# Kernel optimization log

Hardware: AMD Instinct MI355X
Metric: run time of the kernel (lower is better)

## Reference

```python
import jax, jax.numpy as jnp
import numpy as np

N_NODES = 100000
N_EDGES = 1600000
IN_CH = 128
OUT_CH = 32
HEADS = 2
NEG_SLOPE = 0.2  # GATv2Conv default negative_slope


def setup_inputs() -> dict:
    key = jax.random.key(0)
    ks = jax.random.split(key, 6)
    x = jax.random.normal(ks[0], (N_NODES, IN_CH), dtype=jnp.float32)
    edge_index = jax.random.randint(ks[1], (2, N_EDGES), 0, N_NODES, dtype=jnp.int64)
    s_in = 1.0 / np.sqrt(IN_CH)
    Wl = jax.random.normal(ks[2], (IN_CH, HEADS * OUT_CH), dtype=jnp.float32) * s_in  # lin_l weight
    Wr = jax.random.normal(ks[3], (IN_CH, HEADS * OUT_CH), dtype=jnp.float32) * s_in  # lin_r weight
    bl = jnp.zeros((HEADS * OUT_CH,), dtype=jnp.float32)
    br = jnp.zeros((HEADS * OUT_CH,), dtype=jnp.float32)
    att = jax.random.normal(ks[4], (HEADS, OUT_CH), dtype=jnp.float32) * (1.0 / np.sqrt(OUT_CH))
    bias = jnp.zeros((OUT_CH,), dtype=jnp.float32)  # output bias (concat=False -> size out_channels)
    return {"x": x, "Wl": Wl, "bl": bl, "Wr": Wr, "br": br, "att": att, "bias": bias,
            "edge_index": edge_index}


def _gatv2_layer(x, Wl, bl, Wr, br, att, bias, edge_index):
    N = x.shape[0]
    H, C = att.shape
    # add self loops (GATv2Conv default add_self_loops=True)
    loops = jnp.arange(N, dtype=edge_index.dtype)
    src = jnp.concatenate([edge_index[0], loops])  # [E+N] message sources j
    dst = jnp.concatenate([edge_index[1], loops])  # [E+N] message targets i
    # per-node linear transforms (share_weights=False)
    xl = (x @ Wl + bl).reshape(N, H, C)
    xr = (x @ Wr + br).reshape(N, H, C)
    # GATv2 dynamic attention: a^T LeakyReLU(xl[j] + xr[i])
    h = xl[src] + xr[dst]                                   # [E, H, C]
    e = jnp.einsum('ehc,hc->eh', jax.nn.leaky_relu(h, NEG_SLOPE), att)  # [E, H]
    # segment softmax over incoming edges of each target node
    m = jax.ops.segment_max(e, dst, num_segments=N)         # [N, H]
    a = jnp.exp(e - m[dst])
    denom = jax.ops.segment_sum(a, dst, num_segments=N)     # [N, H]
    alpha = a / (denom[dst] + 1e-16)                        # [E, H]
    # weighted scatter-add of source messages
    out = jax.ops.segment_sum(alpha[:, :, None] * xl[src], dst, num_segments=N)  # [N, H, C]
    out = out.mean(axis=1) + bias                           # concat=False -> head mean
    return jax.nn.silu(out)                                 # activation='silu'


def reference(x, Wl, bl, Wr, br, att, bias, edge_index):
    return _gatv2_layer(x, Wl, bl, Wr, br, att, bias, edge_index)
```

## Files before the change

### kernel.cpp

```cpp
#include <hip/hip_runtime.h>
#include <math.h>

#define BSH 9
#define BMASK ((1 << BSH) - 1)
#define CAP 12288
#define ACH 2048

typedef unsigned int uint;
typedef __attribute__((ext_vector_type(8))) short bf16x8;
typedef __attribute__((ext_vector_type(4))) float f32x4;
typedef __attribute__((ext_vector_type(2))) float f32x2;

static __device__ __forceinline__ unsigned short f2bf(float f) {
    uint u = __float_as_uint(f);
    return (unsigned short)((u + 0x7fffu + ((u >> 16) & 1u)) >> 16);
}

static __device__ __forceinline__ bf16x8 pack8(float4 a, float4 b) {
    uint p0, p1, p2, p3;
    asm("v_cvt_pk_bf16_f32 %0, %1, %2" : "=v"(p0) : "v"(a.x), "v"(a.y));
    asm("v_cvt_pk_bf16_f32 %0, %1, %2" : "=v"(p1) : "v"(a.z), "v"(a.w));
    asm("v_cvt_pk_bf16_f32 %0, %1, %2" : "=v"(p2) : "v"(b.x), "v"(b.y));
    asm("v_cvt_pk_bf16_f32 %0, %1, %2" : "=v"(p3) : "v"(b.z), "v"(b.w));
    uint4 u = make_uint4(p0, p1, p2, p3);
    return *(bf16x8*)&u;
}

static __device__ __forceinline__ f32x2 dec2(uint u) {
    f32x2 r;
    r.x = __uint_as_float(u << 16);
    r.y = __uint_as_float(u & 0xffff0000u);
    return r;
}

static __device__ __forceinline__ f32x2 abs2(f32x2 h) {
    f32x2 r;
    r.x = __uint_as_float(__float_as_uint(h.x) & 0x7fffffffu);
    r.y = __uint_as_float(__float_as_uint(h.y) & 0x7fffffffu);
    return r;
}

static __device__ __forceinline__ float qsum(float p) {
    p += __uint_as_float(__builtin_amdgcn_mov_dpp(__float_as_uint(p), 0xB1, 0xF, 0xF, true));
    p += __uint_as_float(__builtin_amdgcn_mov_dpp(__float_as_uint(p), 0x4E, 0xF, 0xF, true));
    return p;
}

__global__ __launch_bounds__(256) void k_prep(const float* __restrict__ Wl,
                                              const float* __restrict__ Wr,
                                              unsigned short* __restrict__ Wt) {
    __shared__ unsigned short s[16][130];
    int b = blockIdx.x;
    int t = threadIdx.x;
#pragma unroll
    for (int i = 0; i < 8; ++i) {
        int idx = i * 256 + t;
        int kl = idx >> 7;
        int n  = idx & 127;
        int k  = b * 16 + kl;
        float v = (n < 64) ? Wl[k * 64 + n] : Wr[k * 64 + (n - 64)];
        s[kl][n] = f2bf(v);
    }
    __syncthreads();
#pragma unroll
    for (int i = 0; i < 2; ++i) {
        int idx = i * 256 + t;
        int n  = idx >> 2;
        int kg = idx & 3;
        ushort4 v;
        v.x = s[kg * 4 + 0][n]; v.y = s[kg * 4 + 1][n];
        v.z = s[kg * 4 + 2][n]; v.w = s[kg * 4 + 3][n];
        *(ushort4*)(Wt + n * 128 + b * 16 + kg * 4) = v;
    }
}

static __device__ __forceinline__ void gemm_body(
        const float* __restrict__ x, const unsigned short* __restrict__ Wt,
        const float* __restrict__ bl, const float* __restrict__ br,
        unsigned short* __restrict__ xlh, float* __restrict__ xr, int N, int bid)
{
    const int t = threadIdx.x;
    const int base = bid * 128;
    const int w = t >> 6;
    const int lo = t & 15;
    const int hi = (t & 63) >> 4;
    int row0 = base + w * 32 + lo;
    int row1 = row0 + 16;
    const float4* x40 = (const float4*)x + (size_t)(row0 < N ? row0 : N - 1) * 32;
    const float4* x41 = (const float4*)x + (size_t)(row1 < N ? row1 : N - 1) * 32;

    f32x4 acc[2][8];
#pragma unroll
    for (int f = 0; f < 2; ++f)
#pragma unroll
        for (int j = 0; j < 8; ++j)
            acc[f][j] = (f32x4){0.f, 0.f, 0.f, 0.f};

#pragma unroll
    for (int ks = 0; ks < 4; ++ks) {
        int f4 = ks * 8 + hi * 2;
        int kofs = ks * 32 + hi * 8;
        bf16x8 av[2], bv[8];
        av[0] = pack8(x40[f4], x40[f4 + 1]);
        av[1] = pack8(x41[f4], x41[f4 + 1]);
#pragma unroll
        for (int j = 0; j < 8; ++j) {
            int nn = j * 16 + lo;
            bv[j] = *(const bf16x8*)(Wt + nn * 128 + kofs);
        }
#pragma unroll
        for (int f = 0; f < 2; ++f)
#pragma unroll
            for (int j = 0; j < 8; ++j)
                acc[f][j] = __builtin_amdgcn_mfma_f32_16x16x32_bf16(av[f], bv[j], acc[f][j], 0, 0, 0);
    }

#pragma unroll
    for (int f = 0; f < 2; ++f) {
        int rbase = base + w * 32 + f * 16 + hi * 4;
#pragma unroll
        for (int j = 0; j < 8; ++j) {
            int nn = j * 16 + lo;
            float bvv = (j < 4) ? bl[nn] : br[nn - 64];
            float vv[4] = {acc[f][j][0] + bvv, acc[f][j][1] + bvv,
                           acc[f][j][2] + bvv, acc[f][j][3] + bvv};
            if (j < 4) {
#pragma unroll
                for (int q = 0; q < 4; ++q)
                    if (rbase + q < N) xlh[(size_t)(rbase + q) * 64 + nn] = f2bf(vv[q]);
            } else {
#pragma unroll
                for (int q = 0; q < 4; ++q)
                    if (rbase + q < N) xr[(size_t)(rbase + q) * 64 + (nn - 64)] = vv[q];
            }
        }
    }
}

static __device__ __forceinline__ void scatA_body(
        const int* __restrict__ ei, int* __restrict__ bcur,
        unsigned* __restrict__ pairs, int E, int T, int NB, int bid)
{
    __shared__ int h[256];
    __shared__ int basem[256];
    int b0 = bid * ACH;
    int cnt = min(ACH, T - b0);
    h[threadIdx.x] = 0;
    __syncthreads();
    for (int i = threadIdx.x; i < cnt; i += 256) {
        int t = b0 + i;
        int d = (t < E) ? ei[E + t] : (t - E);
        atomicAdd(&h[d >> BSH], 1);
    }
    __syncthreads();
    if (threadIdx.x < NB) {
        int c = h[threadIdx.x];
        basem[threadIdx.x] = c ? (threadIdx.x * CAP + atomicAdd(&bcur[threadIdx.x], c)) : 0;
    }
    __syncthreads();
    h[threadIdx.x] = 0;
    __syncthreads();
    for (int i = threadIdx.x; i < cnt; i += 256) {
        int t = b0 + i;
        int s, d;
        if (t < E) { s = ei[t]; d = ei[E + t]; } else { s = t - E; d = s; }
        int b = d >> BSH;
        int idx = atomicAdd(&h[b], 1);
        pairs[basem[b] + idx] = ((unsigned)s << BSH) | (unsigned)(d & BMASK);
    }
}

__global__ __launch_bounds__(256) void k_gs(const float* __restrict__ x,
        const unsigned short* __restrict__ Wt,
        const float* __restrict__ bl, const float* __restrict__ br,
        unsigned short* __restrict__ xlh, float* __restrict__ xr, int N,
        const int* __restrict__ ei, int* __restrict__ bcur,
        unsigned* __restrict__ pairs, int E, int T, int NB, int GB)
{
    if ((int)blockIdx.x < GB)
        gemm_body(x, Wt, bl, br, xlh, xr, N, blockIdx.x);
    else
        scatA_body(ei, bcur, pairs, E, T, NB, blockIdx.x - GB);
}

__global__ __launch_bounds__(512) void k_scatB(const unsigned* __restrict__ pairs,
                                               const int* __restrict__ bcur,
                                               int* __restrict__ src_s, int2* __restrict__ rowrng, int N) {
    __shared__ int cnt[512];
    __shared__ int sm[512];
    __shared__ int lofs[512];
    int b = blockIdx.x;
    int beg = b * CAP, end = beg + bcur[b];
    int nbase = b << BSH;
    cnt[threadIdx.x] = 0;
    __syncthreads();
    for (int i = beg + threadIdx.x; i < end; i += 512)
        atomicAdd(&cnt[pairs[i] & BMASK], 1);
    __syncthreads();
    int v = cnt[threadIdx.x];
    sm[threadIdx.x] = v;
    __syncthreads();
    int acc = v;
    for (int off = 1; off < 512; off <<= 1) {
        int t = (threadIdx.x >= off) ? sm[threadIdx.x - off] : 0;
        __syncthreads();
        acc += t;
        sm[threadIdx.x] = acc;
        __syncthreads();
    }
    int excl = acc - v;
    lofs[threadIdx.x] = excl;
    int n = nbase + threadIdx.x;
    if (n < N) rowrng[n] = make_int2(beg + excl, beg + excl + v);
    cnt[threadIdx.x] = 0;
    __syncthreads();
    for (int i = beg + threadIdx.x; i < end; i += 512) {
        unsigned p = pairs[i];
        int dl = p & BMASK;
        int idx = atomicAdd(&cnt[dl], 1);
        src_s[beg + lofs[dl] + idx] = p >> BSH;
    }
}

__global__ __launch_bounds__(256) void k_fused(const int2* __restrict__ rowrng,
        const int* __restrict__ src_s, const unsigned short* __restrict__ xlh,
        const float* __restrict__ xr, const float* __restrict__ att,
        const float* __restrict__ bias, float* __restrict__ out, int N)
{
    int n = blockIdx.x * 32 + (threadIdx.x >> 3);
    int j = threadIdx.x & 7;
    if (n >= N) return;
    const uint4* xl4 = (const uint4*)xlh + j;
    f32x2 xr2[4], a06[4], a04[4];
    {
        float4 a = ((const float4*)xr)[(size_t)n * 16 + j * 2];
        float4 b = ((const float4*)xr)[(size_t)n * 16 + j * 2 + 1];
        xr2[0] = (f32x2){a.x, a.y}; xr2[1] = (f32x2){a.z, a.w};
        xr2[2] = (f32x2){b.x, b.y}; xr2[3] = (f32x2){b.z, b.w};
        float4 c = ((const float4*)att)[j * 2];
        float4 d = ((const float4*)att)[j * 2 + 1];
        a06[0] = (f32x2){0.6f * c.x, 0.6f * c.y}; a06[1] = (f32x2){0.6f * c.z, 0.6f * c.w};
        a06[2] = (f32x2){0.6f * d.x, 0.6f * d.y}; a06[3] = (f32x2){0.6f * d.z, 0.6f * d.w};
        a04[0] = (f32x2){0.4f * c.x, 0.4f * c.y}; a04[1] = (f32x2){0.4f * c.z, 0.4f * c.w};
        a04[2] = (f32x2){0.4f * d.x, 0.4f * d.y}; a04[3] = (f32x2){0.4f * d.z, 0.4f * d.w};
    }
    int2 rr = rowrng[n];
    float ssum = 0.f;
    f32x2 acc2[4] = {(f32x2){0.f,0.f}, (f32x2){0.f,0.f}, (f32x2){0.f,0.f}, (f32x2){0.f,0.f}};

#define EDGE_BODY(u)                                                      \
    {                                                                     \
        f32x2 v0 = dec2((u).x), v1 = dec2((u).y), v2 = dec2((u).z), v3 = dec2((u).w); \
        f32x2 h0 = v0 + xr2[0], h1 = v1 + xr2[1], h2 = v2 + xr2[2], h3 = v3 + xr2[3]; \
        f32x2 pa = h0 * a06[0]; pa += h1 * a06[1]; pa += h2 * a06[2]; pa += h3 * a06[3]; \
        pa += abs2(h0) * a04[0]; pa += abs2(h1) * a04[1];                 \
        pa += abs2(h2) * a04[2]; pa += abs2(h3) * a04[3];                 \
        float p = pa.x + pa.y;                                            \
        p = qsum(p);                                                      \
        float wq = __expf(p);                                             \
        ssum += wq;                                                       \
        f32x2 ws = (f32x2){wq, wq};                                       \
        acc2[0] += ws * v0; acc2[1] += ws * v1;                           \
        acc2[2] += ws * v2; acc2[3] += ws * v3;                           \
    }

    int i = rr.x;
    for (; i + 8 <= rr.y; i += 8) {
        uint4 u[8];
#pragma unroll
        for (int q = 0; q < 8; ++q)
            u[q] = xl4[((uint)src_s[i + q] << 3)];
#pragma unroll
        for (int q = 0; q < 8; ++q)
            EDGE_BODY(u[q]);
    }
    if (i + 4 <= rr.y) {
        uint4 u[4];
#pragma unroll
        for (int q = 0; q < 4; ++q)
            u[q] = xl4[((uint)src_s[i + q] << 3)];
#pragma unroll
        for (int q = 0; q < 4; ++q)
            EDGE_BODY(u[q]);
        i += 4;
    }
    for (; i < rr.y; ++i) {
        uint4 u0 = xl4[((uint)src_s[i] << 3)];
        EDGE_BODY(u0);
    }
#undef EDGE_BODY

    float inv = 1.f / ssum;
    float o[8];
#pragma unroll
    for (int q = 0; q < 4; ++q) {
        float vx = acc2[q].x * inv, vy = acc2[q].y * inv;
        o[2 * q]     = (vx + __shfl_xor(vx, 4)) * 0.5f;
        o[2 * q + 1] = (vy + __shfl_xor(vy, 4)) * 0.5f;
    }
    if (j < 4) {
        float4 b0 = ((const float4*)bias)[j * 2];
        float4 b1 = ((const float4*)bias)[j * 2 + 1];
        float4 r0, r1;
        r0.x = o[0] + b0.x; r0.y = o[1] + b0.y; r0.z = o[2] + b0.z; r0.w = o[3] + b0.w;
        r1.x = o[4] + b1.x; r1.y = o[5] + b1.y; r1.z = o[6] + b1.z; r1.w = o[7] + b1.w;
        r0.x = r0.x / (1.f + __expf(-r0.x));
        r0.y = r0.y / (1.f + __expf(-r0.y));
        r0.z = r0.z / (1.f + __expf(-r0.z));
        r0.w = r0.w / (1.f + __expf(-r0.w));
        r1.x = r1.x / (1.f + __expf(-r1.x));
        r1.y = r1.y / (1.f + __expf(-r1.y));
        r1.z = r1.z / (1.f + __expf(-r1.z));
        r1.w = r1.w / (1.f + __expf(-r1.w));
        ((float4*)out)[(size_t)n * 8 + j * 2] = r0;
        ((float4*)out)[(size_t)n * 8 + j * 2 + 1] = r1;
    }
}

extern "C" void kernel_launch(void* const* d_in, const int* in_sizes, int n_in,
                              void* d_out, int out_size, void* d_ws, size_t ws_size,
                              hipStream_t stream) {
    const float* x    = (const float*)d_in[0];
    const float* Wl   = (const float*)d_in[1];
    const float* bl   = (const float*)d_in[2];
    const float* Wr   = (const float*)d_in[3];
    const float* br   = (const float*)d_in[4];
    const float* att  = (const float*)d_in[5];
    const float* bias = (const float*)d_in[6];
    const int*   ei   = (const int*)d_in[7];
    float* out = (float*)d_out;

    const int N = in_sizes[0] / 128;
    const int E = in_sizes[7] / 2;
    const int T = E + N;
    const int NB = (N + (1 << BSH) - 1) >> BSH;

    char* p = (char*)d_ws;
    auto take = [&](size_t bytes) {
        char* r = p;
        p += (bytes + 255) & ~(size_t)255;
        return r;
    };
    unsigned short* xlh = (unsigned short*)take((size_t)N * 64 * 2);
    float*    xr     = (float*)take((size_t)N * 64 * 4);
    unsigned* pairs  = (unsigned*)take((size_t)NB * CAP * 4);
    int*      src_s  = (int*)take((size_t)NB * CAP * 4);
    int2*     rowrng = (int2*)take((size_t)N * 8);
    int*      bcur   = (int*)take((size_t)NB * 4);
    unsigned short* Wt = (unsigned short*)take((size_t)128 * 128 * 2);

    const int GB = (N + 127) / 128;
    const int SB = (T + ACH - 1) / ACH;
    hipMemsetAsync(bcur, 0, (size_t)NB * 4, stream);
    k_prep <<<8,             256, 0, stream>>>(Wl, Wr, Wt);
    k_gs   <<<GB + SB,       256, 0, stream>>>(x, Wt, bl, br, xlh, xr, N,
                                               ei, bcur, pairs, E, T, NB, GB);
    k_scatB<<<NB,            512, 0, stream>>>(pairs, bcur, src_s, rowrng, N);
    k_fused<<<(N + 31) / 32, 256, 0, stream>>>(rowrng, src_s, xlh, xr, att, bias, out, N);
}
```

Measured before the change: 121.9 us.

## Store xr in bf16, pre-swizzle weights for MFMA fragments, nontemporal x loads

```diff
diff --git a/kernel.cpp b/kernel.cpp
--- a/kernel.cpp
+++ b/kernel.cpp
@@ -16,7 +16,7 @@
     return (unsigned short)((u + 0x7fffu + ((u >> 16) & 1u)) >> 16);
 }
 
-static __device__ __forceinline__ bf16x8 pack8(float4 a, float4 b) {
+static __device__ __forceinline__ bf16x8 pack8(f32x4 a, f32x4 b) {
     uint p0, p1, p2, p3;
     asm("v_cvt_pk_bf16_f32 %0, %1, %2" : "=v"(p0) : "v"(a.x), "v"(a.y));
     asm("v_cvt_pk_bf16_f32 %0, %1, %2" : "=v"(p1) : "v"(a.z), "v"(a.w));
@@ -49,35 +49,30 @@
 __global__ __launch_bounds__(256) void k_prep(const float* __restrict__ Wl,
                                               const float* __restrict__ Wr,
                                               unsigned short* __restrict__ Wt) {
-    __shared__ unsigned short s[16][130];
-    int b = blockIdx.x;
-    int t = threadIdx.x;
-#pragma unroll
-    for (int i = 0; i < 8; ++i) {
-        int idx = i * 256 + t;
-        int kl = idx >> 7;
-        int n  = idx & 127;
-        int k  = b * 16 + kl;
-        float v = (n < 64) ? Wl[k * 64 + n] : Wr[k * 64 + (n - 64)];
-        s[kl][n] = f2bf(v);
-    }
-    __syncthreads();
-#pragma unroll
-    for (int i = 0; i < 2; ++i) {
-        int idx = i * 256 + t;
-        int n  = idx >> 2;
-        int kg = idx & 3;
-        ushort4 v;
-        v.x = s[kg * 4 + 0][n]; v.y = s[kg * 4 + 1][n];
-        v.z = s[kg * 4 + 2][n]; v.w = s[kg * 4 + 3][n];
-        *(ushort4*)(Wt + n * 128 + b * 16 + kg * 4) = v;
-    }
+    int si = blockIdx.x * 256 + threadIdx.x;
+    int lo = si & 15;
+    int hi = (si >> 4) & 3;
+    int j  = (si >> 6) & 7;
+    int ks = si >> 9;
+    int n  = j * 16 + lo;
+    int kb = ks * 32 + hi * 8;
+    const float* Wp = (n < 64) ? (Wl + n) : (Wr + (n - 64));
+    unsigned short v[8];
+#pragma unroll
+    for (int m = 0; m < 8; ++m)
+        v[m] = f2bf(Wp[(size_t)(kb + m) * 64]);
+    uint4 pk;
+    pk.x = (uint)v[0] | ((uint)v[1] << 16);
+    pk.y = (uint)v[2] | ((uint)v[3] << 16);
+    pk.z = (uint)v[4] | ((uint)v[5] << 16);
+    pk.w = (uint)v[6] | ((uint)v[7] << 16);
+    *(uint4*)(Wt + (size_t)si * 8) = pk;
 }
 
 static __device__ __forceinline__ void gemm_body(
         const float* __restrict__ x, const unsigned short* __restrict__ Wt,
         const float* __restrict__ bl, const float* __restrict__ br,
-        unsigned short* __restrict__ xlh, float* __restrict__ xr, int N, int bid)
+        unsigned short* __restrict__ xlh, unsigned short* __restrict__ xrh, int N, int bid)
 {
     const int t = threadIdx.x;
     const int base = bid * 128;
@@ -86,8 +81,9 @@
     const int hi = (t & 63) >> 4;
     int row0 = base + w * 32 + lo;
     int row1 = row0 + 16;
-    const float4* x40 = (const float4*)x + (size_t)(row0 < N ? row0 : N - 1) * 32;
-    const float4* x41 = (const float4*)x + (size_t)(row1 < N ? row1 : N - 1) * 32;
+    const f32x4* x40 = (const f32x4*)x + (size_t)(row0 < N ? row0 : N - 1) * 32;
+    const f32x4* x41 = (const f32x4*)x + (size_t)(row1 < N ? row1 : N - 1) * 32;
+    const bf16x8* Wf = (const bf16x8*)Wt;
 
     f32x4 acc[2][8];
 #pragma unroll
@@ -99,15 +95,15 @@
 #pragma unroll
     for (int ks = 0; ks < 4; ++ks) {
         int f4 = ks * 8 + hi * 2;
-        int kofs = ks * 32 + hi * 8;
+        int sbase = ks * 512 + hi * 16 + lo;
         bf16x8 av[2], bv[8];
-        av[0] = pack8(x40[f4], x40[f4 + 1]);
-        av[1] = pack8(x41[f4], x41[f4 + 1]);
-#pragma unroll
-        for (int j = 0; j < 8; ++j) {
-            int nn = j * 16 + lo;
-            bv[j] = *(const bf16x8*)(Wt + nn * 128 + kofs);
-        }
+        av[0] = pack8(__builtin_nontemporal_load(x40 + f4),
+                      __builtin_nontemporal_load(x40 + f4 + 1));
+        av[1] = pack8(__builtin_nontemporal_load(x41 + f4),
+                      __builtin_nontemporal_load(x41 + f4 + 1));
+#pragma unroll
+        for (int j = 0; j < 8; ++j)
+            bv[j] = Wf[sbase + j * 64];
 #pragma unroll
         for (int f = 0; f < 2; ++f)
 #pragma unroll
@@ -122,17 +118,10 @@
         for (int j = 0; j < 8; ++j) {
             int nn = j * 16 + lo;
             float bvv = (j < 4) ? bl[nn] : br[nn - 64];
-            float vv[4] = {acc[f][j][0] + bvv, acc[f][j][1] + bvv,
-                           acc[f][j][2] + bvv, acc[f][j][3] + bvv};
-            if (j < 4) {
-#pragma unroll
-                for (int q = 0; q < 4; ++q)
-                    if (rbase + q < N) xlh[(size_t)(rbase + q) * 64 + nn] = f2bf(vv[q]);
-            } else {
-#pragma unroll
-                for (int q = 0; q < 4; ++q)
-                    if (rbase + q < N) xr[(size_t)(rbase + q) * 64 + (nn - 64)] = vv[q];
-            }
+            unsigned short* dst = (j < 4) ? (xlh + nn) : (xrh + (nn - 64));
+#pragma unroll
+            for (int q = 0; q < 4; ++q)
+                if (rbase + q < N) dst[(size_t)(rbase + q) * 64] = f2bf(acc[f][j][q] + bvv);
         }
     }
 }
@@ -173,12 +162,12 @@
 __global__ __launch_bounds__(256) void k_gs(const float* __restrict__ x,
         const unsigned short* __restrict__ Wt,
         const float* __restrict__ bl, const float* __restrict__ br,
-        unsigned short* __restrict__ xlh, float* __restrict__ xr, int N,
+        unsigned short* __restrict__ xlh, unsigned short* __restrict__ xrh, int N,
         const int* __restrict__ ei, int* __restrict__ bcur,
         unsigned* __restrict__ pairs, int E, int T, int NB, int GB)
 {
     if ((int)blockIdx.x < GB)
-        gemm_body(x, Wt, bl, br, xlh, xr, N, blockIdx.x);
+        gemm_body(x, Wt, bl, br, xlh, xrh, N, blockIdx.x);
     else
         scatA_body(ei, bcur, pairs, E, T, NB, blockIdx.x - GB);
 }
@@ -224,7 +213,7 @@
 
 __global__ __launch_bounds__(256) void k_fused(const int2* __restrict__ rowrng,
         const int* __restrict__ src_s, const unsigned short* __restrict__ xlh,
-        const float* __restrict__ xr, const float* __restrict__ att,
+        const unsigned short* __restrict__ xrh, const float* __restrict__ att,
         const float* __restrict__ bias, float* __restrict__ out, int N)
 {
     int n = blockIdx.x * 32 + (threadIdx.x >> 3);
@@ -233,10 +222,9 @@
     const uint4* xl4 = (const uint4*)xlh + j;
     f32x2 xr2[4], a06[4], a04[4];
     {
-        float4 a = ((const float4*)xr)[(size_t)n * 16 + j * 2];
-        float4 b = ((const float4*)xr)[(size_t)n * 16 + j * 2 + 1];
-        xr2[0] = (f32x2){a.x, a.y}; xr2[1] = (f32x2){a.z, a.w};
-        xr2[2] = (f32x2){b.x, b.y}; xr2[3] = (f32x2){b.z, b.w};
+        uint4 u = ((const uint4*)xrh)[(size_t)n * 8 + j];
+        xr2[0] = dec2(u.x); xr2[1] = dec2(u.y);
+        xr2[2] = dec2(u.z); xr2[3] = dec2(u.w);
         float4 c = ((const float4*)att)[j * 2];
         float4 d = ((const float4*)att)[j * 2 + 1];
         a06[0] = (f32x2){0.6f * c.x, 0.6f * c.y}; a06[1] = (f32x2){0.6f * c.z, 0.6f * c.w};
@@ -342,7 +330,7 @@
         return r;
     };
     unsigned short* xlh = (unsigned short*)take((size_t)N * 64 * 2);
-    float*    xr     = (float*)take((size_t)N * 64 * 4);
+    unsigned short* xrh = (unsigned short*)take((size_t)N * 64 * 2);
     unsigned* pairs  = (unsigned*)take((size_t)NB * CAP * 4);
     int*      src_s  = (int*)take((size_t)NB * CAP * 4);
     int2*     rowrng = (int2*)take((size_t)N * 8);
@@ -353,8 +341,8 @@
     const int SB = (T + ACH - 1) / ACH;
     hipMemsetAsync(bcur, 0, (size_t)NB * 4, stream);
     k_prep <<<8,             256, 0, stream>>>(Wl, Wr, Wt);
-    k_gs   <<<GB + SB,       256, 0, stream>>>(x, Wt, bl, br, xlh, xr, N,
+    k_gs   <<<GB + SB,       256, 0, stream>>>(x, Wt, bl, br, xlh, xrh, N,
                                                ei, bcur, pairs, E, T, NB, GB);
     k_scatB<<<NB,            512, 0, stream>>>(pairs, bcur, src_s, rowrng, N);
-    k_fused<<<(N + 31) / 32, 256, 0, stream>>>(rowrng, src_s, xlh, xr, att, bias, out, N);
-}
+    k_fused<<<(N + 31) / 32, 256, 0, stream>>>(rowrng, src_s, xlh, xrh, att, bias, out, N);
+}
```

New measurement: 118.6 us. -2.7%, faster.
